# Kernel optimization log

Measured on AMD Instinct MI355X. Metric: run time of the kernel, lower is better.

The kernel has to match this reference:

```python
import jax, jax.numpy as jnp
import numpy as np

N_HEADS = 8
EPS = 1e-5

def _mha(q_in, kv_in, wq, bq, wk, bk, wv, bv, wo, bo, causal):
    B, N, D = q_in.shape
    Dh = D // N_HEADS
    # projections (weights stored [in, out])
    Q = (q_in @ wq + bq).reshape(B, N, N_HEADS, Dh).swapaxes(1, 2)  # [B,H,N,Dh]
    K = (kv_in @ wk + bk).reshape(B, N, N_HEADS, Dh).swapaxes(1, 2)
    V = (kv_in @ wv + bv).reshape(B, N, N_HEADS, Dh).swapaxes(1, 2)
    scores = jnp.einsum('bhqd,bhkd->bhqk', Q, K) / jnp.sqrt(jnp.asarray(Dh, q_in.dtype))
    if causal:
        m = jnp.triu(jnp.ones((N, N), dtype=bool), k=1)
        scores = jnp.where(m, jnp.asarray(-jnp.inf, scores.dtype), scores)
    w = jax.nn.softmax(scores, axis=-1)
    attn = jnp.einsum('bhqk,bhkd->bhqd', w, V).swapaxes(1, 2).reshape(B, N, D)
    return attn @ wo + bo

def _ln(x, g, b):
    mu = jnp.mean(x, axis=-1, keepdims=True)
    var = jnp.var(x, axis=-1, keepdims=True)
    return (x - mu) / jnp.sqrt(var + EPS) * g + b

def setup_inputs() -> dict:
    key = jax.random.key(0)
    D, H, S = 512, 8, 4
    ks = jax.random.split(key, 32)
    def w(k, shape):
        return jax.random.normal(k, shape, dtype=jnp.float32) * 0.02
    inp = {
        'x': jax.random.normal(ks[0], (2, 2048, D), dtype=jnp.float32),
        'encoder_output': jax.random.normal(ks[1], (2, 2048, D), dtype=jnp.float32),
        # masked self-attention params
        'm_wq': w(ks[2], (D, D)), 'm_bq': jnp.zeros((D,), jnp.float32),
        'm_wk': w(ks[3], (D, D)), 'm_bk': jnp.zeros((D,), jnp.float32),
        'm_wv': w(ks[4], (D, D)), 'm_bv': jnp.zeros((D,), jnp.float32),
        'm_wo': w(ks[5], (D, D)), 'm_bo': jnp.zeros((D,), jnp.float32),
        # cross-attention params
        'c_wq': w(ks[6], (D, D)), 'c_bq': jnp.zeros((D,), jnp.float32),
        'c_wk': w(ks[7], (D, D)), 'c_bk': jnp.zeros((D,), jnp.float32),
        'c_wv': w(ks[8], (D, D)), 'c_bv': jnp.zeros((D,), jnp.float32),
        'c_wo': w(ks[9], (D, D)), 'c_bo': jnp.zeros((D,), jnp.float32),
        # layer norms
        'ln1_g': jnp.ones((D,), jnp.float32), 'ln1_b': jnp.zeros((D,), jnp.float32),
        'ln2_g': jnp.ones((D,), jnp.float32), 'ln2_b': jnp.zeros((D,), jnp.float32),
        'ln3_g': jnp.ones((D,), jnp.float32), 'ln3_b': jnp.zeros((D,), jnp.float32),
        # feed-forward (scale=4)
        'ff_w1': w(ks[10], (D, S * D)), 'ff_b1': jnp.zeros((S * D,), jnp.float32),
        'ff_w2': w(ks[11], (S * D, D)), 'ff_b2': jnp.zeros((D,), jnp.float32),
    }
    return inp

def reference(x, encoder_output,
              m_wq, m_bq, m_wk, m_bk, m_wv, m_bv, m_wo, m_bo,
              c_wq, c_bq, c_wk, c_bk, c_wv, c_bv, c_wo, c_bo,
              ln1_g, ln1_b, ln2_g, ln2_b, ln3_g, ln3_b,
              ff_w1, ff_b1, ff_w2, ff_b2):
    x = _mha(x, x, m_wq, m_bq, m_wk, m_bk, m_wv, m_bv, m_wo, m_bo, causal=True) + x
    x = _ln(x, ln1_g, ln1_b)
    x = _mha(x, encoder_output, c_wq, c_bq, c_wk, c_bk, c_wv, c_bv, c_wo, c_bo, causal=False) + x
    x = _ln(x, ln2_g, ln2_b)
    h = jax.nn.gelu(x @ ff_w1 + ff_b1, approximate=False)  # torch nn.GELU default = exact erf
    x = h @ ff_w2 + ff_b2 + x
    x = _ln(x, ln3_g, ln3_b)
    return x
```

## Files before the change

kernel.cpp:

```cpp
#include <hip/hip_runtime.h>
#include <hip/hip_bf16.h>

typedef __attribute__((ext_vector_type(8))) short short8;
typedef __attribute__((ext_vector_type(4))) float floatx4;
typedef unsigned short u16;
typedef unsigned int u32;

#define QSCALE 0.1803368801111244f

__device__ __forceinline__ u16 f2b(float f) {
    union { float f; u32 u; } v; v.f = f;
    u32 r = v.u + 0x7fffu + ((v.u >> 16) & 1u);
    return (u16)(r >> 16);
}

__device__ __forceinline__ float b2f(u16 b) {
    u32 u = ((u32)b) << 16;
    union { u32 u; float f; } v; v.u = u;
    return v.f;
}

__device__ __forceinline__ u32 pk2(float a, float b) {
    __hip_bfloat162 w = __float22bfloat162_rn(make_float2(a, b));
    return *(u32*)&w;
}

__device__ __forceinline__ void gload(const u16* g, u16* l) {
    __builtin_amdgcn_global_load_lds((const __attribute__((address_space(1))) void*)g,
                                     (__attribute__((address_space(3))) void*)l, 16, 0, 0);
}

struct TPent { const float* s; u16* d; int O; int dI; };
struct TP16 { TPent e[16]; };
__global__ __launch_bounds__(256) void transpose_convert16(TP16 p) {
    __shared__ float t[32][33];
    TPent e = p.e[blockIdx.z];
    int o0 = blockIdx.x * 32, i0 = blockIdx.y * 32;
    int tx = threadIdx.x, ty = threadIdx.y;
#pragma unroll
    for (int k = 0; k < 32; k += 8) t[ty + k][tx] = e.s[(size_t)(i0 + ty + k) * e.O + o0 + tx];
    __syncthreads();
#pragma unroll
    for (int k = 0; k < 32; k += 8) e.d[(size_t)(o0 + ty + k) * e.dI + i0 + tx] = f2b(t[tx][ty + k]);
}

__global__ __launch_bounds__(256) void gather_bias(const float* b0, const float* b1, const float* b2,
                                                   const float* b3, const float* b4,
                                                   float* dqkv, float* dkv) {
    int i = blockIdx.x * 256 + threadIdx.x;
    if      (i < 512)  dqkv[i] = b0[i];
    else if (i < 1024) dqkv[i] = b1[i - 512];
    else if (i < 1536) dqkv[i] = b2[i - 1024];
    else if (i < 2048) dkv[i - 1536] = b3[i - 1536];
    else               dkv[i - 1536] = b4[i - 2048];
}

__global__ __launch_bounds__(256) void cvt_bf16_2(const float4* __restrict__ s0, ushort4* __restrict__ d0,
                                                  const float4* __restrict__ s1, ushort4* __restrict__ d1) {
    int i = blockIdx.x * 256 + threadIdx.x;
    float4 v = s0[i];
    ushort4 o; o.x = f2b(v.x); o.y = f2b(v.y); o.z = f2b(v.z); o.w = f2b(v.w);
    d0[i] = o;
    v = s1[i];
    o.x = f2b(v.x); o.y = f2b(v.y); o.z = f2b(v.z); o.w = f2b(v.w);
    d1[i] = o;
}

__global__ __launch_bounds__(256) void gemm64x128(
    const u16* __restrict__ A, int lda,
    const u16* __restrict__ B, int ldb,
    int K,
    const float* __restrict__ bias,
    const float* __restrict__ residual,
    float* __restrict__ out_f, u16* __restrict__ out_b,
    int out_stride, int scale_ncols, int gelu_flag)
{
    __shared__ u16 lA[64 * 64];
    __shared__ u16 lB[128 * 64];
    int tid = threadIdx.x, wave = tid >> 6, lane = tid & 63;
    int g4 = lane >> 4, c16 = lane & 15;
    int swz = (c16 & 7) << 3;
    int bm = blockIdx.x * 64, bn = blockIdx.y * 128;
    int wm = (wave >> 1) * 32, wn = (wave & 1) * 64;
    int srow = tid >> 3, skseg = ((tid & 7) * 8) ^ ((srow & 7) << 3);
    const u16* Ar = A + (size_t)(bm + srow) * lda + skseg;
    const u16* Br = B + (size_t)(bn + srow) * ldb + skseg;
    size_t a32 = (size_t)32 * lda, b32 = (size_t)32 * ldb;

    floatx4 acc[2][4];
#pragma unroll
    for (int i = 0; i < 2; i++)
#pragma unroll
        for (int j = 0; j < 4; j++) acc[i][j] = (floatx4){0.f, 0.f, 0.f, 0.f};

    for (int kt = 0; kt < K; kt += 64) {
        __syncthreads();
        gload(Ar + kt,           lA + wave * 512);
        gload(Ar + kt + a32,     lA + 2048 + wave * 512);
        gload(Br + kt,           lB + wave * 512);
        gload(Br + kt + b32,     lB + 2048 + wave * 512);
        gload(Br + kt + 2 * b32, lB + 4096 + wave * 512);
        gload(Br + kt + 3 * b32, lB + 6144 + wave * 512);
        __syncthreads();
        short8 aF[2][2], bF[2][4];
#pragma unroll
        for (int kk = 0; kk < 2; kk++) {
            int ko = (g4 * 8 + kk * 32) ^ swz;
#pragma unroll
            for (int i = 0; i < 2; i++) aF[kk][i] = *(const short8*)&lA[(wm + i * 16 + c16) * 64 + ko];
#pragma unroll
            for (int j = 0; j < 4; j++) bF[kk][j] = *(const short8*)&lB[(wn + j * 16 + c16) * 64 + ko];
        }
#pragma unroll
        for (int kk = 0; kk < 2; kk++)
#pragma unroll
            for (int i = 0; i < 2; i++)
#pragma unroll
                for (int j = 0; j < 4; j++)
                    acc[i][j] = __builtin_amdgcn_mfma_f32_16x16x32_bf16(aF[kk][i], bF[kk][j], acc[i][j], 0, 0, 0);
    }

#pragma unroll
    for (int i = 0; i < 2; i++) {
        int row0 = bm + wm + i * 16 + g4 * 4;
#pragma unroll
        for (int j = 0; j < 4; j++) {
            int col = bn + wn + j * 16 + c16;
            float bv = bias[col];
#pragma unroll
            for (int r = 0; r < 4; r++) {
                int row = row0 + r;
                float v = acc[i][j][r] + bv;
                if (col < scale_ncols) v *= QSCALE;
                if (gelu_flag) v = 0.5f * v * (1.f + erff(v * 0.70710678118654752f));
                if (residual) v += residual[(size_t)row * out_stride + col];
                if (out_f) out_f[(size_t)row * out_stride + col] = v;
                else       out_b[(size_t)row * out_stride + col] = f2b(v);
            }
        }
    }
}

__global__ __launch_bounds__(256) void gemm64x128_dual(
    const u16* __restrict__ A0, const u16* __restrict__ B0, const float* __restrict__ bias0,
    u16* __restrict__ out0, int ostride0, int scale0,
    const u16* __restrict__ A1, const u16* __restrict__ B1, const float* __restrict__ bias1,
    u16* __restrict__ out1, int ostride1,
    int ys, int K, int lda, int ldb)
{
    __shared__ u16 lA[64 * 64];
    __shared__ u16 lB[128 * 64];
    int tid = threadIdx.x, wave = tid >> 6, lane = tid & 63;
    int g4 = lane >> 4, c16 = lane & 15;
    int swz = (c16 & 7) << 3;
    int by = blockIdx.y;
    const u16* A; const u16* B; const float* bias; u16* out; int ostride, scaleN, bn;
    if (by < ys) { A = A0; B = B0; bias = bias0; out = out0; ostride = ostride0; scaleN = scale0; bn = by * 128; }
    else         { A = A1; B = B1; bias = bias1; out = out1; ostride = ostride1; scaleN = 0;      bn = (by - ys) * 128; }
    int bm = blockIdx.x * 64;
    int wm = (wave >> 1) * 32, wn = (wave & 1) * 64;
    int srow = tid >> 3, skseg = ((tid & 7) * 8) ^ ((srow & 7) << 3);
    const u16* Ar = A + (size_t)(bm + srow) * lda + skseg;
    const u16* Br = B + (size_t)(bn + srow) * ldb + skseg;
    size_t a32 = (size_t)32 * lda, b32 = (size_t)32 * ldb;

    floatx4 acc[2][4];
#pragma unroll
    for (int i = 0; i < 2; i++)
#pragma unroll
        for (int j = 0; j < 4; j++) acc[i][j] = (floatx4){0.f, 0.f, 0.f, 0.f};

    for (int kt = 0; kt < K; kt += 64) {
        __syncthreads();
        gload(Ar + kt,           lA + wave * 512);
        gload(Ar + kt + a32,     lA + 2048 + wave * 512);
        gload(Br + kt,           lB + wave * 512);
        gload(Br + kt + b32,     lB + 2048 + wave * 512);
        gload(Br + kt + 2 * b32, lB + 4096 + wave * 512);
        gload(Br + kt + 3 * b32, lB + 6144 + wave * 512);
        __syncthreads();
        short8 aF[2][2], bF[2][4];
#pragma unroll
        for (int kk = 0; kk < 2; kk++) {
            int ko = (g4 * 8 + kk * 32) ^ swz;
#pragma unroll
            for (int i = 0; i < 2; i++) aF[kk][i] = *(const short8*)&lA[(wm + i * 16 + c16) * 64 + ko];
#pragma unroll
            for (int j = 0; j < 4; j++) bF[kk][j] = *(const short8*)&lB[(wn + j * 16 + c16) * 64 + ko];
        }
#pragma unroll
        for (int kk = 0; kk < 2; kk++)
#pragma unroll
            for (int i = 0; i < 2; i++)
#pragma unroll
                for (int j = 0; j < 4; j++)
                    acc[i][j] = __builtin_amdgcn_mfma_f32_16x16x32_bf16(aF[kk][i], bF[kk][j], acc[i][j], 0, 0, 0);
    }

#pragma unroll
    for (int i = 0; i < 2; i++) {
        int row0 = bm + wm + i * 16 + g4 * 4;
#pragma unroll
        for (int j = 0; j < 4; j++) {
            int col = bn + wn + j * 16 + c16;
            float bv = bias[col];
#pragma unroll
            for (int r = 0; r < 4; r++) {
                float v = acc[i][j][r] + bv;
                if (col < scaleN) v *= QSCALE;
                out[(size_t)(row0 + r) * ostride + col] = f2b(v);
            }
        }
    }
}

__global__ __launch_bounds__(256) void gemm64x64(
    const u16* __restrict__ A, int lda,
    const u16* __restrict__ B, int ldb,
    int K,
    const float* __restrict__ bias,
    u16* __restrict__ out_b,
    int out_stride, int scale_ncols)
{
    __shared__ u16 lA[64 * 64];
    __shared__ u16 lB[64 * 64];
    int tid = threadIdx.x, wave = tid >> 6, lane = tid & 63;
    int g4 = lane >> 4, c16 = lane & 15;
    int swz = (c16 & 7) << 3;
    int bm = blockIdx.x * 64, bn = blockIdx.y * 64;
    int wm = wave * 16;
    int srow = tid >> 3, skseg = ((tid & 7) * 8) ^ ((srow & 7) << 3);
    const u16* Ar = A + (size_t)(bm + srow) * lda + skseg;
    const u16* Br = B + (size_t)(bn + srow) * ldb + skseg;
    size_t a32 = (size_t)32 * lda, b32 = (size_t)32 * ldb;

    floatx4 acc[4];
#pragma unroll
    for (int j = 0; j < 4; j++) acc[j] = (floatx4){0.f, 0.f, 0.f, 0.f};

    for (int kt = 0; kt < K; kt += 64) {
        __syncthreads();
        gload(Ar + kt,       lA + wave * 512);
        gload(Ar + kt + a32, lA + 2048 + wave * 512);
        gload(Br + kt,       lB + wave * 512);
        gload(Br + kt + b32, lB + 2048 + wave * 512);
        __syncthreads();
        short8 aF[2], bF[2][4];
#pragma unroll
        for (int kk = 0; kk < 2; kk++) {
            int ko = (g4 * 8 + kk * 32) ^ swz;
            aF[kk] = *(const short8*)&lA[(wm + c16) * 64 + ko];
#pragma unroll
            for (int j = 0; j < 4; j++) bF[kk][j] = *(const short8*)&lB[(j * 16 + c16) * 64 + ko];
        }
#pragma unroll
        for (int kk = 0; kk < 2; kk++)
#pragma unroll
            for (int j = 0; j < 4; j++)
                acc[j] = __builtin_amdgcn_mfma_f32_16x16x32_bf16(aF[kk], bF[kk][j], acc[j], 0, 0, 0);
    }

    int row0 = bm + wm + g4 * 4;
#pragma unroll
    for (int j = 0; j < 4; j++) {
        int col = bn + j * 16 + c16;
        float bv = bias[col];
#pragma unroll
        for (int r = 0; r < 4; r++) {
            int row = row0 + r;
            float v = acc[j][r] + bv;
            if (col < scale_ncols) v *= QSCALE;
            out_b[(size_t)row * out_stride + col] = f2b(v);
        }
    }
}

__global__ __launch_bounds__(256) void gemm64x64s(
    const u16* __restrict__ A, int lda,
    const u16* __restrict__ B, int ldb,
    int Ksub,
    const float* __restrict__ bias,
    const float* __restrict__ res_f,
    const u16* __restrict__ res_b,
    u16* __restrict__ out0, int out_stride)
{
    __shared__ u16 lA[64 * 64];
    __shared__ u16 lB[64 * 64];
    int tid = threadIdx.x, wave = tid >> 6, lane = tid & 63;
    int g4 = lane >> 4, c16 = lane & 15;
    int swz = (c16 & 7) << 3;
    int bm = blockIdx.x * 64, bn = blockIdx.y * 64, sp = blockIdx.z;
    int wm = wave * 16;
    int srow = tid >> 3;
    int skseg = (((tid & 7) * 8) ^ ((srow & 7) << 3)) + sp * Ksub;
    const u16* Ar = A + (size_t)(bm + srow) * lda + skseg;
    const u16* Br = B + (size_t)(bn + srow) * ldb + skseg;
    size_t a32 = (size_t)32 * lda, b32 = (size_t)32 * ldb;

    floatx4 acc[4];
#pragma unroll
    for (int j = 0; j < 4; j++) acc[j] = (floatx4){0.f, 0.f, 0.f, 0.f};

    for (int kt = 0; kt < Ksub; kt += 64) {
        __syncthreads();
        gload(Ar + kt,       lA + wave * 512);
        gload(Ar + kt + a32, lA + 2048 + wave * 512);
        gload(Br + kt,       lB + wave * 512);
        gload(Br + kt + b32, lB + 2048 + wave * 512);
        __syncthreads();
        short8 aF[2], bF[2][4];
#pragma unroll
        for (int kk = 0; kk < 2; kk++) {
            int ko = (g4 * 8 + kk * 32) ^ swz;
            aF[kk] = *(const short8*)&lA[(wm + c16) * 64 + ko];
#pragma unroll
            for (int j = 0; j < 4; j++) bF[kk][j] = *(const short8*)&lB[(j * 16 + c16) * 64 + ko];
        }
#pragma unroll
        for (int kk = 0; kk < 2; kk++)
#pragma unroll
            for (int j = 0; j < 4; j++)
                acc[j] = __builtin_amdgcn_mfma_f32_16x16x32_bf16(aF[kk], bF[kk][j], acc[j], 0, 0, 0);
    }

    u16* out = out0 + (size_t)sp * 4096 * 512;
    int row0 = bm + wm + g4 * 4;
#pragma unroll
    for (int j = 0; j < 4; j++) {
        int col = bn + j * 16 + c16;
        float bv = (sp == 0) ? bias[col] : 0.f;
#pragma unroll
        for (int r = 0; r < 4; r++) {
            int row = row0 + r;
            float v = acc[j][r] + bv;
            if (sp == 0) {
                if (res_f)      v += res_f[(size_t)row * out_stride + col];
                else if (res_b) v += b2f(res_b[(size_t)row * out_stride + col]);
            }
            out[(size_t)row * out_stride + col] = f2b(v);
        }
    }
}

__global__ __launch_bounds__(256) void attn_fused(
    const u16* __restrict__ Qp, int q_stride,
    const u16* __restrict__ Kp, int kv_stride,
    const u16* __restrict__ Vp,
    u16* __restrict__ Opart,
    float* __restrict__ Lpart,
    int causal)
{
    __shared__ u16 lK[64 * 72];
    __shared__ u16 lVT[64 * 72];
    int tid = threadIdx.x, wave = tid >> 6, lane = tid & 63;
    int g4 = lane >> 4, c16 = lane & 15;
    int id = blockIdx.x;
    int bh = (id & 7) | ((id >> 3 & 1) << 3);
    int rest = id >> 4;
    int qt = rest & 31;
    int sp = rest >> 5;
    if (causal) qt = 31 - qt;
    size_t rowbase = (size_t)(bh >> 3) * 2048;
    int hoff = (bh & 7) * 64;
    const u16* Q = Qp + rowbase * q_stride + hoff;
    const u16* K = Kp + rowbase * kv_stride + hoff;
    const u16* V = Vp + rowbase * kv_stride + hoff;

    int qrow0 = qt * 64 + wave * 16;
    short8 qf0 = *(const short8*)&Q[(size_t)(qrow0 + c16) * q_stride + g4 * 8];
    short8 qf1 = *(const short8*)&Q[(size_t)(qrow0 + c16) * q_stride + g4 * 8 + 32];

    int kr = tid >> 2, ks = (tid & 3) * 16;
    int krow = 16 * (2 * (kr >> 5) + ((kr >> 2) & 1)) + 4 * ((kr >> 3) & 3) + (kr & 3);
    const u16* Kbase = K + (size_t)kr * kv_stride + ks;
    int vk0 = (tid >> 3) * 2, vs = (tid & 7) * 8;
    const u16* Vbase = V + (size_t)vk0 * kv_stride + vs;

    int4 kv0, kv1, vv0, vv1;
    auto load_tile = [&](int kt) {
        const u16* kp = Kbase + (size_t)kt * 64 * kv_stride;
        kv0 = *(const int4*)(kp);
        kv1 = *(const int4*)(kp + 8);
        const u16* vp = Vbase + (size_t)kt * 64 * kv_stride;
        vv0 = *(const int4*)(vp);
        vv1 = *(const int4*)(vp + kv_stride);
    };
    auto store_tile = [&]() {
        *(int4*)&lK[krow * 72 + ks] = kv0;
        *(int4*)&lK[krow * 72 + ks + 8] = kv1;
        const u16* pa = (const u16*)&vv0;
        const u16* pb = (const u16*)&vv1;
#pragma unroll
        for (int j = 0; j < 8; j++) {
            int dh = vs + j;
            int keyS = vk0 ^ (((dh >> 3) & 3) << 4);
            u32 w = (u32)pa[j] | ((u32)pb[j] << 16);
            *(u32*)&lVT[dh * 72 + keyS] = w;
        }
    };

    floatx4 o_acc[4];
#pragma unroll
    for (int d = 0; d < 4; d++) o_acc[d] = (floatx4){0.f, 0.f, 0.f, 0.f};
    float lsum = 0.f;

    int ktend = causal ? (qt + 1) : 32;
    int kt = sp;
    if (kt < ktend) load_tile(kt);

    for (; kt < ktend; kt += 2) {
        __syncthreads();
        store_tile();
        __syncthreads();
        if (kt + 2 < ktend) load_tile(kt + 2);

        floatx4 sc[4];
#pragma unroll
        for (int nt = 0; nt < 4; nt++) {
            short8 b0 = *(const short8*)&lK[(nt * 16 + c16) * 72 + g4 * 8];
            short8 b1 = *(const short8*)&lK[(nt * 16 + c16) * 72 + g4 * 8 + 32];
            floatx4 z = (floatx4){0.f, 0.f, 0.f, 0.f};
            z = __builtin_amdgcn_mfma_f32_16x16x32_bf16(b0, qf0, z, 0, 0, 0);
            z = __builtin_amdgcn_mfma_f32_16x16x32_bf16(b1, qf1, z, 0, 0, 0);
            sc[nt] = z;
        }
        if (causal && kt == qt) {
            int qr = qt * 64 + wave * 16 + c16;
#pragma unroll
            for (int nt = 0; nt < 4; nt++) {
                int key0 = kt * 64 + 8 * g4 + 4 * (nt & 1) + 32 * (nt >> 1);
#pragma unroll
                for (int r = 0; r < 4; r++)
                    if (key0 + r > qr) sc[nt][r] = -1e30f;
            }
        }
        float e[4][4];
#pragma unroll
        for (int nt = 0; nt < 4; nt++) {
#pragma unroll
            for (int r = 0; r < 4; r++) {
                e[nt][r] = exp2f(sc[nt][r]);
                lsum += e[nt][r];
            }
        }
        short8 pa0, pa1;
        {
            u32 w[8];
            w[0] = pk2(e[0][0], e[0][1]); w[1] = pk2(e[0][2], e[0][3]);
            w[2] = pk2(e[1][0], e[1][1]); w[3] = pk2(e[1][2], e[1][3]);
            w[4] = pk2(e[2][0], e[2][1]); w[5] = pk2(e[2][2], e[2][3]);
            w[6] = pk2(e[3][0], e[3][1]); w[7] = pk2(e[3][2], e[3][3]);
            pa0 = *(short8*)&w[0];
            pa1 = *(short8*)&w[4];
        }
#pragma unroll
        for (int d = 0; d < 4; d++) {
            int swz = ((2 * d + (c16 >> 3)) & 3) << 4;
            short8 vb0 = *(const short8*)&lVT[(d * 16 + c16) * 72 + ((g4 * 8) ^ swz)];
            short8 vb1 = *(const short8*)&lVT[(d * 16 + c16) * 72 + ((32 + g4 * 8) ^ swz)];
            o_acc[d] = __builtin_amdgcn_mfma_f32_16x16x32_bf16(pa0, vb0, o_acc[d], 0, 0, 0);
            o_acc[d] = __builtin_amdgcn_mfma_f32_16x16x32_bf16(pa1, vb1, o_acc[d], 0, 0, 0);
        }
    }

    lsum += __shfl_xor(lsum, 16);
    lsum += __shfl_xor(lsum, 32);
    size_t slab = (size_t)(sp * 16 + bh) * 2048;
    if (g4 == 0) Lpart[slab + qrow0 + c16] = lsum;
    u16* Ob = Opart + (slab + qrow0) * 64;
#pragma unroll
    for (int d = 0; d < 4; d++)
#pragma unroll
        for (int r = 0; r < 4; r++)
            Ob[(size_t)(4 * g4 + r) * 64 + d * 16 + c16] = f2b(o_acc[d][r]);
}

__global__ __launch_bounds__(256) void attn_combine(
    const ushort4* __restrict__ Op,
    const float* __restrict__ Lp,
    ushort4* __restrict__ out)
{
    int e = blockIdx.x * 256 + threadIdx.x;
    int dh4 = e & 15;
    int qrow = (e >> 4) & 2047;
    int bh = e >> 15;
    int li = bh * 2048 + qrow;
    float l = Lp[li] + Lp[32768 + li];
    float inv = 1.f / l;
    ushort4 a = Op[e];
    ushort4 b = Op[524288 + e];
    ushort4 o;
    o.x = f2b((b2f(a.x) + b2f(b.x)) * inv);
    o.y = f2b((b2f(a.y) + b2f(b.y)) * inv);
    o.z = f2b((b2f(a.z) + b2f(b.z)) * inv);
    o.w = f2b((b2f(a.w) + b2f(b.w)) * inv);
    int row = (bh >> 3) * 2048 + qrow;
    out[(size_t)row * 128 + (bh & 7) * 16 + dh4] = o;
}

__global__ __launch_bounds__(256) void ln_kernel(const u16* __restrict__ in0,
                                                 const u16* __restrict__ in1,
                                                 const float* __restrict__ g,
                                                 const float* __restrict__ b,
                                                 float* __restrict__ out_f,
                                                 u16* __restrict__ out_b)
{
    const int D = 512;
    int row = blockIdx.x, tid = threadIdx.x;
    size_t base = (size_t)row * D;
    float v0 = b2f(in0[base + tid]) + b2f(in1[base + tid]);
    float v1 = b2f(in0[base + tid + 256]) + b2f(in1[base + tid + 256]);
    float s = v0 + v1, ss = v0 * v0 + v1 * v1;
#pragma unroll
    for (int off = 1; off < 64; off <<= 1) { s += __shfl_xor(s, off); ss += __shfl_xor(ss, off); }
    __shared__ float red[8];
    int wave = tid >> 6, lane = tid & 63;
    if (lane == 0) { red[wave] = s; red[4 + wave] = ss; }
    __syncthreads();
    float st = red[0] + red[1] + red[2] + red[3];
    float sst = red[4] + red[5] + red[6] + red[7];
    float mu = st * (1.f / 512.f);
    float var = sst * (1.f / 512.f) - mu * mu;
    float rs = rsqrtf(var + 1e-5f);
    float y0 = (v0 - mu) * rs * g[tid] + b[tid];
    float y1 = (v1 - mu) * rs * g[tid + 256] + b[tid + 256];
    if (out_f) { out_f[base + tid] = y0; out_f[base + tid + 256] = y1; }
    if (out_b) { out_b[base + tid] = f2b(y0); out_b[base + tid + 256] = f2b(y1); }
}

extern "C" void kernel_launch(void* const* d_in, const int* in_sizes, int n_in,
                              void* d_out, int out_size, void* d_ws, size_t ws_size,
                              hipStream_t stream)
{
    (void)in_sizes; (void)n_in; (void)out_size; (void)ws_size;
    const float* x     = (const float*)d_in[0];
    const float* enc   = (const float*)d_in[1];
    const float* m_wq  = (const float*)d_in[2];  const float* m_bq = (const float*)d_in[3];
    const float* m_wk  = (const float*)d_in[4];  const float* m_bk = (const float*)d_in[5];
    const float* m_wv  = (const float*)d_in[6];  const float* m_bv = (const float*)d_in[7];
    const float* m_wo  = (const float*)d_in[8];  const float* m_bo = (const float*)d_in[9];
    const float* c_wq  = (const float*)d_in[10]; const float* c_bq = (const float*)d_in[11];
    const float* c_wk  = (const float*)d_in[12]; const float* c_bk = (const float*)d_in[13];
    const float* c_wv  = (const float*)d_in[14]; const float* c_bv = (const float*)d_in[15];
    const float* c_wo  = (const float*)d_in[16]; const float* c_bo = (const float*)d_in[17];
    const float* ln1_g = (const float*)d_in[18]; const float* ln1_b = (const float*)d_in[19];
    const float* ln2_g = (const float*)d_in[20]; const float* ln2_b = (const float*)d_in[21];
    const float* ln3_g = (const float*)d_in[22]; const float* ln3_b = (const float*)d_in[23];
    const float* ff_w1 = (const float*)d_in[24]; const float* ff_b1 = (const float*)d_in[25];
    const float* ff_w2 = (const float*)d_in[26]; const float* ff_b2 = (const float*)d_in[27];

    char* base = (char*)d_ws; size_t off = 0;
    auto alloc = [&](size_t bytes) -> void* {
        void* p = base + off; off = (off + bytes + 255) & ~(size_t)255; return p;
    };
    u16*   Wqkv_m = (u16*)alloc(1536 * 512 * 2);
    u16*   Wo_m   = (u16*)alloc(512 * 512 * 2);
    u16*   Wq_c   = (u16*)alloc(512 * 512 * 2);
    u16*   Wkv_c  = (u16*)alloc(1024 * 512 * 2);
    u16*   Wo_c   = (u16*)alloc(512 * 512 * 2);
    u16*   W1t    = (u16*)alloc(2048 * 512 * 2);
    u16*   W2t    = (u16*)alloc(512 * 2048 * 2);
    float* bqkv_m = (float*)alloc(1536 * 4);
    float* bkv_c  = (float*)alloc(1024 * 4);
    u16*   xb     = (u16*)alloc((size_t)4096 * 512 * 2);
    u16*   encb   = (u16*)alloc((size_t)4096 * 512 * 2);
    u16*   qkvm   = (u16*)alloc((size_t)4096 * 1536 * 2);
    u16*   attnm  = (u16*)alloc((size_t)4096 * 512 * 2);
    u16*   y01    = (u16*)alloc((size_t)2 * 4096 * 512 * 2);
    u16*   x1b    = (u16*)alloc((size_t)4096 * 512 * 2);
    u16*   qc     = (u16*)alloc((size_t)4096 * 512 * 2);
    u16*   kvc    = (u16*)alloc((size_t)4096 * 1024 * 2);
    u16*   attnc  = (u16*)alloc((size_t)4096 * 512 * 2);
    u16*   x2b    = (u16*)alloc((size_t)4096 * 512 * 2);
    u16*   h      = (u16*)alloc((size_t)4096 * 2048 * 2);
    u16*   Opart  = (u16*)alloc((size_t)2 * 16 * 2048 * 64 * 2);
    float* Lpart  = (float*)alloc((size_t)2 * 16 * 2048 * 4);

    TP16 tp;
    tp.e[0] = {m_wq, Wqkv_m,              512, 512};
    tp.e[1] = {m_wk, Wqkv_m + 512 * 512,  512, 512};
    tp.e[2] = {m_wv, Wqkv_m + 1024 * 512, 512, 512};
    tp.e[3] = {m_wo, Wo_m,                512, 512};
    tp.e[4] = {c_wq, Wq_c,                512, 512};
    tp.e[5] = {c_wk, Wkv_c,               512, 512};
    tp.e[6] = {c_wv, Wkv_c + 512 * 512,   512, 512};
    tp.e[7] = {c_wo, Wo_c,                512, 512};
    for (int k = 0; k < 4; k++)
        tp.e[8 + k]  = {ff_w1 + 512 * k,        W1t + k * 512 * 512, 2048, 512};
    for (int k = 0; k < 4; k++)
        tp.e[12 + k] = {ff_w2 + (size_t)512 * k * 512, W2t + 512 * k, 512, 2048};
    transpose_convert16<<<dim3(16, 16, 16), dim3(32, 8), 0, stream>>>(tp);
    gather_bias<<<10, 256, 0, stream>>>(m_bq, m_bk, m_bv, c_bk, c_bv, bqkv_m, bkv_c);
    cvt_bf16_2<<<2048, 256, 0, stream>>>((const float4*)x, (ushort4*)xb,
                                         (const float4*)enc, (ushort4*)encb);

    gemm64x128_dual<<<dim3(64, 20), 256, 0, stream>>>(
        xb, Wqkv_m, bqkv_m, qkvm, 1536, 512,
        encb, Wkv_c, bkv_c, kvc, 1024,
        12, 512, 512, 512);

    attn_fused<<<1024, 256, 0, stream>>>(qkvm, 1536, qkvm + 512, 1536, qkvm + 1024,
                                         Opart, Lpart, 1);
    attn_combine<<<2048, 256, 0, stream>>>((const ushort4*)Opart, Lpart, (ushort4*)attnm);
    gemm64x64s<<<dim3(64, 8, 2), 256, 0, stream>>>(attnm, 512, Wo_m, 512, 256,
                                                   m_bo, x, nullptr, y01, 512);
    ln_kernel<<<4096, 256, 0, stream>>>(y01, y01 + (size_t)4096 * 512, ln1_g, ln1_b,
                                        nullptr, x1b);

    gemm64x64<<<dim3(64, 8), 256, 0, stream>>>(x1b, 512, Wq_c, 512, 512,
                                               c_bq, qc, 512, 512);
    attn_fused<<<1024, 256, 0, stream>>>(qc, 512, kvc, 1024, kvc + 512,
                                         Opart, Lpart, 0);
    attn_combine<<<2048, 256, 0, stream>>>((const ushort4*)Opart, Lpart, (ushort4*)attnc);
    gemm64x64s<<<dim3(64, 8, 2), 256, 0, stream>>>(attnc, 512, Wo_c, 512, 256,
                                                   c_bo, nullptr, x1b, y01, 512);
    ln_kernel<<<4096, 256, 0, stream>>>(y01, y01 + (size_t)4096 * 512, ln2_g, ln2_b,
                                        nullptr, x2b);

    gemm64x128<<<dim3(64, 16), 256, 0, stream>>>(x2b, 512, W1t, 512, 512,
                                                 ff_b1, nullptr, nullptr, h, 2048, 0, 1);
    gemm64x64s<<<dim3(64, 8, 2), 256, 0, stream>>>(h, 2048, W2t, 2048, 1024,
                                                   ff_b2, nullptr, x2b, y01, 512);
    ln_kernel<<<4096, 256, 0, stream>>>(y01, y01 + (size_t)4096 * 512, ln3_g, ln3_b,
                                        (float*)d_out, nullptr);
}
```

Baseline: 299.7 us.

## Pair causal query tiles per block and split attention KV four ways

Causal self-attention now gives each block two query tiles, p and 31-p, so every block walks the same 33 KV tiles. Those tiles are split four ways across blocks, which evens out the triangular workload that was unbalanced under the old two-way split. Cross-attention also moves to a four-way KV split, doubling the block count to 2048 with half the tiles per block. The combine kernel now sums four partial outputs and denominators, which costs more partial-buffer traffic and extra per-block setup and Q loads.

```diff
diff --git a/kernel.cpp b/kernel.cpp
--- a/kernel.cpp
+++ b/kernel.cpp
@@ -342,13 +342,12 @@
     }
 }
 
-__global__ __launch_bounds__(256) void attn_fused(
+__global__ __launch_bounds__(256, 4) void attn_causal_paired(
     const u16* __restrict__ Qp, int q_stride,
     const u16* __restrict__ Kp, int kv_stride,
     const u16* __restrict__ Vp,
     u16* __restrict__ Opart,
-    float* __restrict__ Lpart,
-    int causal)
+    float* __restrict__ Lpart)
 {
     __shared__ u16 lK[64 * 72];
     __shared__ u16 lVT[64 * 72];
@@ -357,18 +356,21 @@
     int id = blockIdx.x;
     int bh = (id & 7) | ((id >> 3 & 1) << 3);
     int rest = id >> 4;
-    int qt = rest & 31;
-    int sp = rest >> 5;
-    if (causal) qt = 31 - qt;
+    int p = rest & 15;
+    int sp = rest >> 4;
+    int qtA = p, qtB = 31 - p;
     size_t rowbase = (size_t)(bh >> 3) * 2048;
     int hoff = (bh & 7) * 64;
     const u16* Q = Qp + rowbase * q_stride + hoff;
     const u16* K = Kp + rowbase * kv_stride + hoff;
     const u16* V = Vp + rowbase * kv_stride + hoff;
 
-    int qrow0 = qt * 64 + wave * 16;
-    short8 qf0 = *(const short8*)&Q[(size_t)(qrow0 + c16) * q_stride + g4 * 8];
-    short8 qf1 = *(const short8*)&Q[(size_t)(qrow0 + c16) * q_stride + g4 * 8 + 32];
+    int qrowA = qtA * 64 + wave * 16;
+    int qrowB = qtB * 64 + wave * 16;
+    short8 qa0 = *(const short8*)&Q[(size_t)(qrowA + c16) * q_stride + g4 * 8];
+    short8 qa1 = *(const short8*)&Q[(size_t)(qrowA + c16) * q_stride + g4 * 8 + 32];
+    short8 qb0 = *(const short8*)&Q[(size_t)(qrowB + c16) * q_stride + g4 * 8];
+    short8 qb1 = *(const short8*)&Q[(size_t)(qrowB + c16) * q_stride + g4 * 8 + 32];
 
     int kr = tid >> 2, ks = (tid & 3) * 16;
     int krow = 16 * (2 * (kr >> 5) + ((kr >> 2) & 1)) + 4 * ((kr >> 3) & 3) + (kr & 3);
@@ -399,21 +401,13 @@
         }
     };
 
-    floatx4 o_acc[4];
-#pragma unroll
-    for (int d = 0; d < 4; d++) o_acc[d] = (floatx4){0.f, 0.f, 0.f, 0.f};
-    float lsum = 0.f;
-
-    int ktend = causal ? (qt + 1) : 32;
-    int kt = sp;
-    if (kt < ktend) load_tile(kt);
-
-    for (; kt < ktend; kt += 2) {
-        __syncthreads();
-        store_tile();
-        __syncthreads();
-        if (kt + 2 < ktend) load_tile(kt + 2);
-
+    floatx4 oA[4], oB[4];
+#pragma unroll
+    for (int d = 0; d < 4; d++) { oA[d] = (floatx4){0.f,0.f,0.f,0.f}; oB[d] = (floatx4){0.f,0.f,0.f,0.f}; }
+    float lsA = 0.f, lsB = 0.f;
+
+    auto compute_tile = [&](short8 qf0, short8 qf1, floatx4 (&oacc)[4], float& lsum,
+                            bool diag, int qtile, int kt) {
         floatx4 sc[4];
 #pragma unroll
         for (int nt = 0; nt < 4; nt++) {
@@ -424,8 +418,8 @@
             z = __builtin_amdgcn_mfma_f32_16x16x32_bf16(b1, qf1, z, 0, 0, 0);
             sc[nt] = z;
         }
-        if (causal && kt == qt) {
-            int qr = qt * 64 + wave * 16 + c16;
+        if (diag) {
+            int qr = qtile * 64 + wave * 16 + c16;
 #pragma unroll
             for (int nt = 0; nt < 4; nt++) {
                 int key0 = kt * 64 + 8 * g4 + 4 * (nt & 1) + 32 * (nt >> 1);
@@ -436,13 +430,14 @@
         }
         float e[4][4];
 #pragma unroll
-        for (int nt = 0; nt < 4; nt++) {
-#pragma unroll
-            for (int r = 0; r < 4; r++) {
-                e[nt][r] = exp2f(sc[nt][r]);
-                lsum += e[nt][r];
-            }
-        }
+        for (int nt = 0; nt < 4; nt++)
+#pragma unroll
+            for (int r = 0; r < 4; r++) e[nt][r] = exp2f(sc[nt][r]);
+        float s0 = (e[0][0] + e[0][1]) + (e[0][2] + e[0][3]);
+        float s1 = (e[1][0] + e[1][1]) + (e[1][2] + e[1][3]);
+        float s2 = (e[2][0] + e[2][1]) + (e[2][2] + e[2][3]);
+        float s3 = (e[3][0] + e[3][1]) + (e[3][2] + e[3][3]);
+        lsum += (s0 + s1) + (s2 + s3);
         short8 pa0, pa1;
         {
             u32 w[8];
@@ -455,6 +450,143 @@
         }
 #pragma unroll
         for (int d = 0; d < 4; d++) {
+            int vswz = ((2 * d + (c16 >> 3)) & 3) << 4;
+            short8 vb0 = *(const short8*)&lVT[(d * 16 + c16) * 72 + ((g4 * 8) ^ vswz)];
+            short8 vb1 = *(const short8*)&lVT[(d * 16 + c16) * 72 + ((32 + g4 * 8) ^ vswz)];
+            oacc[d] = __builtin_amdgcn_mfma_f32_16x16x32_bf16(pa0, vb0, oacc[d], 0, 0, 0);
+            oacc[d] = __builtin_amdgcn_mfma_f32_16x16x32_bf16(pa1, vb1, oacc[d], 0, 0, 0);
+        }
+    };
+
+    int t = sp;
+    load_tile(t <= p ? t : t - p - 1);
+    for (; t < 33; t += 4) {
+        __syncthreads();
+        store_tile();
+        __syncthreads();
+        if (t + 4 < 33) { int tn = t + 4; load_tile(tn <= p ? tn : tn - p - 1); }
+        if (t <= p) compute_tile(qa0, qa1, oA, lsA, t == p,  qtA, t);
+        else        compute_tile(qb0, qb1, oB, lsB, t == 32, qtB, t - p - 1);
+    }
+
+    lsA += __shfl_xor(lsA, 16); lsA += __shfl_xor(lsA, 32);
+    lsB += __shfl_xor(lsB, 16); lsB += __shfl_xor(lsB, 32);
+    size_t slab = (size_t)(sp * 16 + bh) * 2048;
+    if (g4 == 0) {
+        Lpart[slab + qrowA + c16] = lsA;
+        Lpart[slab + qrowB + c16] = lsB;
+    }
+    u16* ObA = Opart + (slab + qrowA) * 64;
+    u16* ObB = Opart + (slab + qrowB) * 64;
+#pragma unroll
+    for (int d = 0; d < 4; d++)
+#pragma unroll
+        for (int r = 0; r < 4; r++) {
+            ObA[(size_t)(4 * g4 + r) * 64 + d * 16 + c16] = f2b(oA[d][r]);
+            ObB[(size_t)(4 * g4 + r) * 64 + d * 16 + c16] = f2b(oB[d][r]);
+        }
+}
+
+__global__ __launch_bounds__(256) void attn_fused(
+    const u16* __restrict__ Qp, int q_stride,
+    const u16* __restrict__ Kp, int kv_stride,
+    const u16* __restrict__ Vp,
+    u16* __restrict__ Opart,
+    float* __restrict__ Lpart)
+{
+    __shared__ u16 lK[64 * 72];
+    __shared__ u16 lVT[64 * 72];
+    int tid = threadIdx.x, wave = tid >> 6, lane = tid & 63;
+    int g4 = lane >> 4, c16 = lane & 15;
+    int id = blockIdx.x;
+    int bh = (id & 7) | ((id >> 3 & 1) << 3);
+    int rest = id >> 4;
+    int qt = rest & 31;
+    int sp = rest >> 5;
+    size_t rowbase = (size_t)(bh >> 3) * 2048;
+    int hoff = (bh & 7) * 64;
+    const u16* Q = Qp + rowbase * q_stride + hoff;
+    const u16* K = Kp + rowbase * kv_stride + hoff;
+    const u16* V = Vp + rowbase * kv_stride + hoff;
+
+    int qrow0 = qt * 64 + wave * 16;
+    short8 qf0 = *(const short8*)&Q[(size_t)(qrow0 + c16) * q_stride + g4 * 8];
+    short8 qf1 = *(const short8*)&Q[(size_t)(qrow0 + c16) * q_stride + g4 * 8 + 32];
+
+    int kr = tid >> 2, ks = (tid & 3) * 16;
+    int krow = 16 * (2 * (kr >> 5) + ((kr >> 2) & 1)) + 4 * ((kr >> 3) & 3) + (kr & 3);
+    const u16* Kbase = K + (size_t)kr * kv_stride + ks;
+    int vk0 = (tid >> 3) * 2, vs = (tid & 7) * 8;
+    const u16* Vbase = V + (size_t)vk0 * kv_stride + vs;
+
+    int4 kv0, kv1, vv0, vv1;
+    auto load_tile = [&](int kt) {
+        const u16* kp = Kbase + (size_t)kt * 64 * kv_stride;
+        kv0 = *(const int4*)(kp);
+        kv1 = *(const int4*)(kp + 8);
+        const u16* vp = Vbase + (size_t)kt * 64 * kv_stride;
+        vv0 = *(const int4*)(vp);
+        vv1 = *(const int4*)(vp + kv_stride);
+    };
+    auto store_tile = [&]() {
+        *(int4*)&lK[krow * 72 + ks] = kv0;
+        *(int4*)&lK[krow * 72 + ks + 8] = kv1;
+        const u16* pa = (const u16*)&vv0;
+        const u16* pb = (const u16*)&vv1;
+#pragma unroll
+        for (int j = 0; j < 8; j++) {
+            int dh = vs + j;
+            int keyS = vk0 ^ (((dh >> 3) & 3) << 4);
+            u32 w = (u32)pa[j] | ((u32)pb[j] << 16);
+            *(u32*)&lVT[dh * 72 + keyS] = w;
+        }
+    };
+
+    floatx4 o_acc[4];
+#pragma unroll
+    for (int d = 0; d < 4; d++) o_acc[d] = (floatx4){0.f, 0.f, 0.f, 0.f};
+    float lsum = 0.f;
+
+    int kt = sp;
+    load_tile(kt);
+    for (; kt < 32; kt += 4) {
+        __syncthreads();
+        store_tile();
+        __syncthreads();
+        if (kt + 4 < 32) load_tile(kt + 4);
+
+        floatx4 sc[4];
+#pragma unroll
+        for (int nt = 0; nt < 4; nt++) {
+            short8 b0 = *(const short8*)&lK[(nt * 16 + c16) * 72 + g4 * 8];
+            short8 b1 = *(const short8*)&lK[(nt * 16 + c16) * 72 + g4 * 8 + 32];
+            floatx4 z = (floatx4){0.f, 0.f, 0.f, 0.f};
+            z = __builtin_amdgcn_mfma_f32_16x16x32_bf16(b0, qf0, z, 0, 0, 0);
+            z = __builtin_amdgcn_mfma_f32_16x16x32_bf16(b1, qf1, z, 0, 0, 0);
+            sc[nt] = z;
+        }
+        float e[4][4];
+#pragma unroll
+        for (int nt = 0; nt < 4; nt++)
+#pragma unroll
+            for (int r = 0; r < 4; r++) e[nt][r] = exp2f(sc[nt][r]);
+        float s0 = (e[0][0] + e[0][1]) + (e[0][2] + e[0][3]);
+        float s1 = (e[1][0] + e[1][1]) + (e[1][2] + e[1][3]);
+        float s2 = (e[2][0] + e[2][1]) + (e[2][2] + e[2][3]);
+        float s3 = (e[3][0] + e[3][1]) + (e[3][2] + e[3][3]);
+        lsum += (s0 + s1) + (s2 + s3);
+        short8 pa0, pa1;
+        {
+            u32 w[8];
+            w[0] = pk2(e[0][0], e[0][1]); w[1] = pk2(e[0][2], e[0][3]);
+            w[2] = pk2(e[1][0], e[1][1]); w[3] = pk2(e[1][2], e[1][3]);
+            w[4] = pk2(e[2][0], e[2][1]); w[5] = pk2(e[2][2], e[2][3]);
+            w[6] = pk2(e[3][0], e[3][1]); w[7] = pk2(e[3][2], e[3][3]);
+            pa0 = *(short8*)&w[0];
+            pa1 = *(short8*)&w[4];
+        }
+#pragma unroll
+        for (int d = 0; d < 4; d++) {
             int swz = ((2 * d + (c16 >> 3)) & 3) << 4;
             short8 vb0 = *(const short8*)&lVT[(d * 16 + c16) * 72 + ((g4 * 8) ^ swz)];
             short8 vb1 = *(const short8*)&lVT[(d * 16 + c16) * 72 + ((32 + g4 * 8) ^ swz)];
@@ -485,15 +617,17 @@
     int qrow = (e >> 4) & 2047;
     int bh = e >> 15;
     int li = bh * 2048 + qrow;
-    float l = Lp[li] + Lp[32768 + li];
+    float l = (Lp[li] + Lp[32768 + li]) + (Lp[65536 + li] + Lp[98304 + li]);
     float inv = 1.f / l;
     ushort4 a = Op[e];
     ushort4 b = Op[524288 + e];
+    ushort4 c = Op[2 * 524288 + e];
+    ushort4 d = Op[3 * 524288 + e];
     ushort4 o;
-    o.x = f2b((b2f(a.x) + b2f(b.x)) * inv);
-    o.y = f2b((b2f(a.y) + b2f(b.y)) * inv);
-    o.z = f2b((b2f(a.z) + b2f(b.z)) * inv);
-    o.w = f2b((b2f(a.w) + b2f(b.w)) * inv);
+    o.x = f2b(((b2f(a.x) + b2f(b.x)) + (b2f(c.x) + b2f(d.x))) * inv);
+    o.y = f2b(((b2f(a.y) + b2f(b.y)) + (b2f(c.y) + b2f(d.y))) * inv);
+    o.z = f2b(((b2f(a.z) + b2f(b.z)) + (b2f(c.z) + b2f(d.z))) * inv);
+    o.w = f2b(((b2f(a.w) + b2f(b.w)) + (b2f(c.w) + b2f(d.w))) * inv);
     int row = (bh >> 3) * 2048 + qrow;
     out[(size_t)row * 128 + (bh & 7) * 16 + dh4] = o;
 }
@@ -573,8 +707,8 @@
     u16*   attnc  = (u16*)alloc((size_t)4096 * 512 * 2);
     u16*   x2b    = (u16*)alloc((size_t)4096 * 512 * 2);
     u16*   h      = (u16*)alloc((size_t)4096 * 2048 * 2);
-    u16*   Opart  = (u16*)alloc((size_t)2 * 16 * 2048 * 64 * 2);
-    float* Lpart  = (float*)alloc((size_t)2 * 16 * 2048 * 4);
+    u16*   Opart  = (u16*)alloc((size_t)4 * 16 * 2048 * 64 * 2);
+    float* Lpart  = (float*)alloc((size_t)4 * 16 * 2048 * 4);
 
     TP16 tp;
     tp.e[0] = {m_wq, Wqkv_m,              512, 512};
@@ -599,8 +733,8 @@
         encb, Wkv_c, bkv_c, kvc, 1024,
         12, 512, 512, 512);
 
-    attn_fused<<<1024, 256, 0, stream>>>(qkvm, 1536, qkvm + 512, 1536, qkvm + 1024,
-                                         Opart, Lpart, 1);
+    attn_causal_paired<<<1024, 256, 0, stream>>>(qkvm, 1536, qkvm + 512, 1536, qkvm + 1024,
+                                                 Opart, Lpart);
     attn_combine<<<2048, 256, 0, stream>>>((const ushort4*)Opart, Lpart, (ushort4*)attnm);
     gemm64x64s<<<dim3(64, 8, 2), 256, 0, stream>>>(attnm, 512, Wo_m, 512, 256,
                                                    m_bo, x, nullptr, y01, 512);
@@ -609,8 +743,8 @@
 
     gemm64x64<<<dim3(64, 8), 256, 0, stream>>>(x1b, 512, Wq_c, 512, 512,
                                                c_bq, qc, 512, 512);
-    attn_fused<<<1024, 256, 0, stream>>>(qc, 512, kvc, 1024, kvc + 512,
-                                         Opart, Lpart, 0);
+    attn_fused<<<2048, 256, 0, stream>>>(qc, 512, kvc, 1024, kvc + 512,
+                                         Opart, Lpart);
     attn_combine<<<2048, 256, 0, stream>>>((const ushort4*)Opart, Lpart, (ushort4*)attnc);
     gemm64x64s<<<dim3(64, 8, 2), 256, 0, stream>>>(attnc, 512, Wo_c, 512, 256,
                                                    c_bo, nullptr, x1b, y01, 512);
```

New measurement: 308.0 us. +2.8%, slower.
